# Optimization experiments

Measured on AMD Instinct MI355X. Metric: run time of the kernel, lower is better.

The kernel has to match this reference:

```python
import jax, jax.numpy as jnp
import numpy as np

B, T, D = 2, 2048, 1024
E, K, FF = 8, 2, 4096


def setup_inputs() -> dict:
    key = jax.random.key(0)
    ks = jax.random.split(key, 4)
    scale = 0.02
    return {
        "x": jax.random.normal(ks[0], (B, T, D), jnp.float32),
        "gate_w": jax.random.normal(ks[1], (D, E), jnp.float32) * scale,
        "gate_b": jnp.zeros((E,), jnp.float32),
        "w1": jax.random.normal(ks[2], (E, D, FF), jnp.float32) * scale,
        "b1": jnp.zeros((E, FF), jnp.float32),
        "w2": jax.random.normal(ks[3], (E, FF, D), jnp.float32) * scale,
        "b2": jnp.zeros((E, D), jnp.float32),
    }


def reference(x, gate_w, gate_b, w1, b1, w2, b2):
    # x: (B,T,D). Original runs every expert densely over all tokens then masks;
    # since mask*x == x at selected positions and output is re-masked, the math
    # equals: output[t] = sum_k softmax(topk_vals)[k] * expert_{idx_k}(x)[t].
    n_experts = w1.shape[0]
    gate_logits = x @ gate_w + gate_b                      # (B,T,E)
    topk_vals, topk_idx = jax.lax.top_k(gate_logits, K)    # (B,T,K)
    topk_w = jax.nn.softmax(topk_vals, axis=-1)            # (B,T,K)
    onehot = jax.nn.one_hot(topk_idx, n_experts, dtype=x.dtype)  # (B,T,K,E)
    comb = jnp.sum(onehot * topk_w[..., None], axis=2)     # (B,T,E) combine weights

    # Dense per-expert FFN over all tokens (faithful to original redundant compute)
    h = jax.nn.gelu(jnp.einsum('btd,edf->ebtf', x, w1) + b1[:, None, None, :],
                    approximate=False)                      # (E,B,T,FF)
    y = jnp.einsum('ebtf,efd->ebtd', h, w2) + b2[:, None, None, :]  # (E,B,T,D)
    output = jnp.einsum('ebtd,bte->btd', y, comb)           # (B,T,D)

    expert_counts = jnp.sum(onehot, axis=(0, 1, 2)).astype(jnp.float32)  # (E,)
    return output, gate_logits, topk_idx, expert_counts
```

## Files before the change

kernel.cpp:

```cpp
#include <hip/hip_runtime.h>
#include <math.h>

#define NTOK 4096
#define DIM  1024
#define NE   8
#define FF   4096

#define OUT_LOGITS 4194304
#define OUT_IDX    4227072
#define OUT_CNT    4235264

typedef unsigned short u16;
typedef __bf16 bf16x8 __attribute__((ext_vector_type(8)));
typedef float  f32x4  __attribute__((ext_vector_type(4)));
typedef u16    u16x8  __attribute__((ext_vector_type(8)));

__device__ __forceinline__ u16 f2bf(float f) {
  union { float f; unsigned u; } v; v.f = f;
  unsigned r = v.u + 0x7fffu + ((v.u >> 16) & 1u);
  return (u16)(r >> 16);
}

__device__ __forceinline__ float gelu_f(float v) {
  float u = v * (0.7978845608f + 0.0356774081f * v * v);
  float e = __expf(2.f * u);
  float t = 1.f - 2.f / (e + 1.f);
  return 0.5f * v * (1.f + t);
}

__device__ __forceinline__ void gload_lds16(const u16* g, u16* l) {
  __builtin_amdgcn_global_load_lds(
      (const __attribute__((address_space(1))) void*)(g),
      (__attribute__((address_space(3))) void*)(l), 16, 0, 0);
}

__global__ __launch_bounds__(256) void transpose_cvt2_kernel(
    const float* __restrict__ w1, u16* __restrict__ w1t,
    const float* __restrict__ w2, u16* __restrict__ w2t) {
  __shared__ float tile[4096];
  int id = blockIdx.x;
  const float* in; u16* out; int R, C, xt, yt, z;
  if (id < 8192) {
    in = w1; out = w1t; R = DIM; C = FF;
    xt = id & 63; yt = (id >> 6) & 15; z = id >> 10;
  } else {
    int i2 = id - 8192;
    in = w2; out = w2t; R = FF; C = DIM;
    xt = i2 & 15; yt = (i2 >> 4) & 63; z = i2 >> 10;
  }
  in  += (size_t)z * R * C;
  out += (size_t)z * R * C;
  const int c0 = xt * 64, r0 = yt * 64;
  const int t = threadIdx.x;

  {
    int cc = t & 15, rr = t >> 4;
    #pragma unroll
    for (int p = 0; p < 4; p++) {
      int r = rr + p * 16;
      float4 v = *(const float4*)(in + (size_t)(r0 + r) * C + c0 + cc * 4);
      *(float4*)&tile[r * 64 + ((cc ^ (r >> 3)) << 2)] = v;
    }
  }
  __syncthreads();
  {
    int h = t & 7, cg = t >> 3;
    #pragma unroll
    for (int p = 0; p < 2; p++) {
      int c = p * 32 + cg;
      int base = ((((c >> 2) ^ h) << 2)) + (c & 3);
      u16x8 o;
      #pragma unroll
      for (int j = 0; j < 8; j++)
        o[j] = f2bf(tile[(h * 8 + j) * 64 + base]);
      *(u16x8*)(out + (size_t)(c0 + c) * R + r0 + h * 8) = o;
    }
  }
}

__global__ __launch_bounds__(256) void gate_kernel(const float* __restrict__ x,
                                                   const float* __restrict__ gw,
                                                   const float* __restrict__ gb,
                                                   float* __restrict__ out,
                                                   int2* __restrict__ tk_idx,
                                                   float2* __restrict__ tk_w) {
  int wave = threadIdx.x >> 6, lane = threadIdx.x & 63;
  int token = blockIdx.x * 4 + wave;
  const float* xr = x + (size_t)token * DIM + lane * 16;
  float acc[NE];
  #pragma unroll
  for (int e = 0; e < NE; e++) acc[e] = 0.f;
  #pragma unroll
  for (int c = 0; c < 16; c += 4) {
    float4 xv = *(const float4*)(xr + c);
    const float* gwr = gw + (size_t)(lane * 16 + c) * NE;
    float xs[4] = {xv.x, xv.y, xv.z, xv.w};
    #pragma unroll
    for (int q = 0; q < 4; q++)
      #pragma unroll
      for (int e = 0; e < NE; e++)
        acc[e] += xs[q] * gwr[q * NE + e];
  }
  #pragma unroll
  for (int off = 32; off; off >>= 1)
    #pragma unroll
    for (int e = 0; e < NE; e++)
      acc[e] += __shfl_down(acc[e], off);

  if (lane == 0) {
    float lg[NE];
    #pragma unroll
    for (int e = 0; e < NE; e++) {
      lg[e] = acc[e] + gb[e];
      out[OUT_LOGITS + token * NE + e] = lg[e];
    }
    int i0 = 0; float v0 = lg[0];
    #pragma unroll
    for (int e = 1; e < NE; e++) if (lg[e] > v0) { v0 = lg[e]; i0 = e; }
    int i1 = -1; float v1 = -1e30f;
    #pragma unroll
    for (int e = 0; e < NE; e++) if (e != i0 && lg[e] > v1) { v1 = lg[e]; i1 = e; }
    float ex = expf(v1 - v0);
    float s = 1.f + ex;
    out[OUT_IDX + token * 2]     = (float)i0;
    out[OUT_IDX + token * 2 + 1] = (float)i1;
    tk_idx[token] = make_int2(i0, i1);
    tk_w[token]   = make_float2(1.f / s, ex / s);
  }
}

__global__ __launch_bounds__(512) void build_lists_kernel(
    const int2* __restrict__ tk_idx, const float2* __restrict__ tk_w,
    int* __restrict__ counts, int* __restrict__ offsets,
    int* __restrict__ tok_list, float* __restrict__ wt_list,
    float* __restrict__ cnt_out) {
  __shared__ int s_cnt[NE];
  int e = threadIdx.x >> 6, lane = threadIdx.x & 63;
  int cnt = 0;
  for (int base = 0; base < NTOK; base += 64) {
    int2 idx = tk_idx[base + lane];
    cnt += __popcll(__ballot(idx.x == e || idx.y == e));
  }
  if (lane == 0) s_cnt[e] = cnt;
  __syncthreads();
  int off = 0;
  for (int ee = 0; ee < e; ee++) off += s_cnt[ee];
  if (lane == 0) {
    counts[e]  = s_cnt[e];
    offsets[e] = off;
    cnt_out[e] = (float)s_cnt[e];
  }
  int pos = off;
  for (int base = 0; base < NTOK; base += 64) {
    int tok = base + lane;
    int2 idx = tk_idx[tok];
    float2 w = tk_w[tok];
    bool m0 = (idx.x == e), m1 = (idx.y == e);
    bool m = m0 || m1;
    unsigned long long mask = __ballot(m);
    if (m) {
      int p = pos + __popcll(mask & ((1ull << lane) - 1ull));
      tok_list[p] = tok;
      wt_list[p]  = m0 ? w.x : w.y;
    }
    pos += __popcll(mask);
  }
}

__global__ __launch_bounds__(256) void gather_x_kernel(const float* __restrict__ x,
                                                       const int* __restrict__ tok_list,
                                                       u16* __restrict__ xg) {
  int g = blockIdx.x;
  int tok = tok_list[g];
  int c = threadIdx.x * 4;
  float4 v = *(const float4*)(x + (size_t)tok * DIM + c);
  ushort4 o;
  o.x = f2bf(v.x); o.y = f2bf(v.y); o.z = f2bf(v.z); o.w = f2bf(v.w);
  *(ushort4*)(xg + (size_t)g * DIM + c) = o;
}

template <int MODE, int BM, int BN>
__global__ __launch_bounds__(512, 2) void moe_gemm2_kernel(
    const u16* __restrict__ Abase, const u16* __restrict__ Bbase,
    const float* __restrict__ bias,
    const int* __restrict__ counts, const int* __restrict__ offsets,
    const int* __restrict__ tok_list, const float* __restrict__ wt_list,
    u16* __restrict__ Hout, float* __restrict__ Out) {
  constexpr int KT = (MODE == 0) ? DIM : FF;
  constexpr int NT = (MODE == 0) ? FF : DIM;
  constexpr int LA = BM / 64;
  constexpr int LB = BN / 64;
  constexpr int MR = BM / 32;
  constexpr int NR = BN / 64;
  constexpr int ASZ = BM * 64;
  constexpr int BSZ = BN * 64;
  constexpr int NTILES = (MODE == 0) ? (KT / 64) : (KT / 128);

  extern __shared__ u16 sm[];

  const int zz = blockIdx.z;
  const int e  = (MODE == 1) ? (zz >> 1) : zz;
  const int koff = (MODE == 1) ? ((zz & 1) * (KT / 2)) : 0;
  const int ne = counts[e];
  const int m0 = blockIdx.y * BM;
  if (m0 >= ne) return;
  const int n0   = blockIdx.x * BN;
  const int offs = offsets[e];

  const int t = threadIdx.x;
  const int wave = t >> 6, lane = t & 63;
  const int quad = lane >> 4, l16 = lane & 15;
  const int wmb = (wave & 1) * (BM / 2);
  const int wnb = (wave >> 1) * (BN / 4);

  const u16* aptr[LA];
  const u16* bptr[LB];
  #pragma unroll
  for (int p = 0; p < LA; p++) {
    int idx = p * 512 + t;
    int row = idx >> 3, c = idx & 7;
    int clog = c ^ (row & 7);
    int s = m0 + row; if (s > ne - 1) s = ne - 1;
    aptr[p] = Abase + (size_t)(offs + s) * KT + koff + clog * 8;
  }
  #pragma unroll
  for (int p = 0; p < LB; p++) {
    int idx = p * 512 + t;
    int row = idx >> 3, c = idx & 7;
    int clog = c ^ (row & 7);
    bptr[p] = Bbase + ((size_t)e * NT + n0 + row) * KT + koff + clog * 8;
  }

  auto stage = [&](int buf, int k0) {
    #pragma unroll
    for (int p = 0; p < LA; p++)
      gload_lds16(aptr[p] + k0, sm + buf * ASZ + (p * 512 + t) * 8);
    #pragma unroll
    for (int p = 0; p < LB; p++)
      gload_lds16(bptr[p] + k0, sm + 2 * ASZ + buf * BSZ + (p * 512 + t) * 8);
  };

  const int xrow = l16 & 7;
  const int xo[2] = { ((0 + quad) ^ xrow) * 8, ((4 + quad) ^ xrow) * 8 };
  const int abase0 = (wmb + l16) * 64;
  const int bbase0 = 2 * ASZ + (wnb + l16) * 64;

  f32x4 acc[MR][NR];
  #pragma unroll
  for (int i = 0; i < MR; i++)
    #pragma unroll
    for (int j = 0; j < NR; j++)
      acc[i][j] = (f32x4){0.f, 0.f, 0.f, 0.f};

  stage(0, 0);
  __syncthreads();
  int cur = 0;
  for (int kt = 0; kt < NTILES; ++kt) {
    if (kt + 1 < NTILES) stage(cur ^ 1, (kt + 1) * 64);
    const u16* As = sm + cur * ASZ;
    const u16* Bs = sm + cur * BSZ;
    #pragma unroll
    for (int kk = 0; kk < 2; kk++) {
      bf16x8 a[MR], b[NR];
      #pragma unroll
      for (int i = 0; i < MR; i++) a[i] = *(const bf16x8*)&As[abase0 + i * 1024 + xo[kk]];
      #pragma unroll
      for (int j = 0; j < NR; j++) b[j] = *(const bf16x8*)&Bs[bbase0 + j * 1024 + xo[kk]];
      #pragma unroll
      for (int i = 0; i < MR; i++)
        #pragma unroll
        for (int j = 0; j < NR; j++)
          acc[i][j] = __builtin_amdgcn_mfma_f32_16x16x32_bf16(a[i], b[j], acc[i][j], 0, 0, 0);
    }
    __syncthreads();
    cur ^= 1;
  }

  if (MODE == 0) {
    const float* bb = bias + (size_t)e * FF + n0 + wnb;
    float bc[NR];
    #pragma unroll
    for (int j = 0; j < NR; j++) bc[j] = bb[j * 16 + l16];
    #pragma unroll
    for (int i = 0; i < MR; i++) {
      #pragma unroll
      for (int r = 0; r < 4; r++) {
        int s = m0 + wmb + i * 16 + quad * 4 + r;
        if (s < ne) {
          u16* hr = Hout + (size_t)(offs + s) * FF + n0 + wnb;
          #pragma unroll
          for (int j = 0; j < NR; j++)
            hr[j * 16 + l16] = f2bf(gelu_f(acc[i][j][r] + bc[j]));
        }
      }
    }
  } else {
    const float* bb = bias + (size_t)e * DIM + n0 + wnb;
    float bc[NR];
    #pragma unroll
    for (int j = 0; j < NR; j++) bc[j] = (zz & 1) ? 0.f : bb[j * 16 + l16];
    #pragma unroll
    for (int i = 0; i < MR; i++) {
      #pragma unroll
      for (int r = 0; r < 4; r++) {
        int s = m0 + wmb + i * 16 + quad * 4 + r;
        if (s < ne) {
          int   tok = tok_list[offs + s];
          float w   = wt_list[offs + s];
          float* orow = Out + (size_t)tok * DIM + n0 + wnb;
          #pragma unroll
          for (int j = 0; j < NR; j++)
            atomicAdd(&orow[j * 16 + l16], (acc[i][j][r] + bc[j]) * w);
        }
      }
    }
  }
}

extern "C" void kernel_launch(void* const* d_in, const int* in_sizes, int n_in,
                              void* d_out, int out_size, void* d_ws, size_t ws_size,
                              hipStream_t stream) {
  const float* x   = (const float*)d_in[0];
  const float* gw  = (const float*)d_in[1];
  const float* gb  = (const float*)d_in[2];
  const float* w1  = (const float*)d_in[3];
  const float* b1  = (const float*)d_in[4];
  const float* w2  = (const float*)d_in[5];
  const float* b2  = (const float*)d_in[6];
  float* out = (float*)d_out;
  char*  ws  = (char*)d_ws;

  u16* w1t = (u16*)(ws);
  u16* w2t = (u16*)(ws + 1ull * 67108864);
  u16* h   = (u16*)(ws + 2ull * 67108864);
  u16* xg  = (u16*)(ws + 3ull * 67108864);
  char* meta = ws + 3ull * 67108864 + 16777216;
  int*    counts   = (int*)(meta);
  int*    offsets  = (int*)(meta + 64);
  int*    tok_list = (int*)(meta + 128);
  float*  wt_list  = (float*)(meta + 128 + 32768);
  int2*   tk_idx   = (int2*)(meta + 128 + 2 * 32768);
  float2* tk_w     = (float2*)(meta + 128 + 2 * 32768 + 32768);
  (void)in_sizes; (void)n_in; (void)out_size; (void)ws_size;

  static bool attr_set = false;
  if (!attr_set) {
    hipFuncSetAttribute(reinterpret_cast<const void*>(moe_gemm2_kernel<0, 256, 256>),
                        hipFuncAttributeMaxDynamicSharedMemorySize, 131072);
    hipFuncSetAttribute(reinterpret_cast<const void*>(moe_gemm2_kernel<1, 128, 256>),
                        hipFuncAttributeMaxDynamicSharedMemorySize, 98304);
    attr_set = true;
  }

  hipMemsetAsync(out, 0, (size_t)OUT_LOGITS * 4, stream);

  transpose_cvt2_kernel<<<16384, 256, 0, stream>>>(w1, w1t, w2, w2t);
  gate_kernel<<<NTOK / 4, 256, 0, stream>>>(x, gw, gb, out, tk_idx, tk_w);
  build_lists_kernel<<<1, 512, 0, stream>>>(tk_idx, tk_w, counts, offsets, tok_list, wt_list,
                                            out + OUT_CNT);
  gather_x_kernel<<<2 * NTOK, 256, 0, stream>>>(x, tok_list, xg);

  moe_gemm2_kernel<0, 256, 256><<<dim3(FF / 256, NTOK / 256, NE), 512, 131072, stream>>>(
      xg, w1t, b1, counts, offsets, tok_list, wt_list, h, nullptr);
  moe_gemm2_kernel<1, 128, 256><<<dim3(DIM / 256, NTOK / 128, NE * 2), 512, 98304, stream>>>(
      h, w2t, b2, counts, offsets, tok_list, wt_list, nullptr, out);
}
```

Baseline: 636.3 us.

## Enlarge transpose tiles, parallelize list building, drop split-K in second GEMM

Three separate changes. The weight transpose/convert kernel now handles 128-row tiles per block, halving the block count. The token-list builder runs one block per expert, with each wave counting a slice of tokens, instead of a single block scanning all tokens serially. The down-projection GEMM no longer splits K across two z-slices, which halves its grid and its atomicAdd traffic but leaves fewer blocks and longer K loops per block.

```diff
diff --git a/kernel.cpp b/kernel.cpp
--- a/kernel.cpp
+++ b/kernel.cpp
@@ -34,29 +34,29 @@
       (__attribute__((address_space(3))) void*)(l), 16, 0, 0);
 }
 
-__global__ __launch_bounds__(256) void transpose_cvt2_kernel(
+__global__ __launch_bounds__(256) void transpose_cvt3_kernel(
     const float* __restrict__ w1, u16* __restrict__ w1t,
     const float* __restrict__ w2, u16* __restrict__ w2t) {
-  __shared__ float tile[4096];
+  __shared__ float tile[8192];
   int id = blockIdx.x;
   const float* in; u16* out; int R, C, xt, yt, z;
-  if (id < 8192) {
+  if (id < 4096) {
     in = w1; out = w1t; R = DIM; C = FF;
-    xt = id & 63; yt = (id >> 6) & 15; z = id >> 10;
+    xt = id & 63; yt = (id >> 6) & 7; z = id >> 9;
   } else {
-    int i2 = id - 8192;
+    int i2 = id - 4096;
     in = w2; out = w2t; R = FF; C = DIM;
-    xt = i2 & 15; yt = (i2 >> 4) & 63; z = i2 >> 10;
+    xt = i2 & 15; yt = (i2 >> 4) & 31; z = i2 >> 9;
   }
   in  += (size_t)z * R * C;
   out += (size_t)z * R * C;
-  const int c0 = xt * 64, r0 = yt * 64;
+  const int c0 = xt * 64, r0 = yt * 128;
   const int t = threadIdx.x;
 
   {
     int cc = t & 15, rr = t >> 4;
     #pragma unroll
-    for (int p = 0; p < 4; p++) {
+    for (int p = 0; p < 8; p++) {
       int r = rr + p * 16;
       float4 v = *(const float4*)(in + (size_t)(r0 + r) * C + c0 + cc * 4);
       *(float4*)&tile[r * 64 + ((cc ^ (r >> 3)) << 2)] = v;
@@ -64,11 +64,12 @@
   }
   __syncthreads();
   {
-    int h = t & 7, cg = t >> 3;
-    #pragma unroll
-    for (int p = 0; p < 2; p++) {
-      int c = p * 32 + cg;
-      int base = ((((c >> 2) ^ h) << 2)) + (c & 3);
+    int h = t & 15, cg = t >> 4;
+    #pragma unroll
+    for (int q = 0; q < 4; q++) {
+      int c = q * 16 + cg;
+      int phys = ((q * 4 + (cg >> 2)) ^ h) << 2;
+      int base = phys + (cg & 3);
       u16x8 o;
       #pragma unroll
       for (int j = 0; j < 8; j++)
@@ -129,39 +130,59 @@
   }
 }
 
-__global__ __launch_bounds__(512) void build_lists_kernel(
+__global__ __launch_bounds__(512) void build_lists8_kernel(
     const int2* __restrict__ tk_idx, const float2* __restrict__ tk_w,
     int* __restrict__ counts, int* __restrict__ offsets,
     int* __restrict__ tok_list, float* __restrict__ wt_list,
     float* __restrict__ cnt_out) {
-  __shared__ int s_cnt[NE];
-  int e = threadIdx.x >> 6, lane = threadIdx.x & 63;
-  int cnt = 0;
-  for (int base = 0; base < NTOK; base += 64) {
-    int2 idx = tk_idx[base + lane];
-    cnt += __popcll(__ballot(idx.x == e || idx.y == e));
-  }
-  if (lane == 0) s_cnt[e] = cnt;
+  __shared__ int s_cnt[8][NE];
+  const int e = blockIdx.x;
+  const int w = threadIdx.x >> 6, lane = threadIdx.x & 63;
+  const int tbase = w * 512;
+  int cnt[NE];
+  #pragma unroll
+  for (int ee = 0; ee < NE; ee++) cnt[ee] = 0;
+  #pragma unroll
+  for (int it = 0; it < 8; it++) {
+    int2 idx = tk_idx[tbase + it * 64 + lane];
+    #pragma unroll
+    for (int ee = 0; ee < NE; ee++)
+      cnt[ee] += __popcll(__ballot(idx.x == ee || idx.y == ee));
+  }
+  if (lane == 0) {
+    #pragma unroll
+    for (int ee = 0; ee < NE; ee++) s_cnt[w][ee] = cnt[ee];
+  }
   __syncthreads();
+  int total[NE];
+  #pragma unroll
+  for (int ee = 0; ee < NE; ee++) {
+    int s = 0;
+    #pragma unroll
+    for (int ww = 0; ww < 8; ww++) s += s_cnt[ww][ee];
+    total[ee] = s;
+  }
   int off = 0;
-  for (int ee = 0; ee < e; ee++) off += s_cnt[ee];
-  if (lane == 0) {
-    counts[e]  = s_cnt[e];
+  for (int ee = 0; ee < e; ee++) off += total[ee];
+  if (threadIdx.x == 0) {
+    counts[e]  = total[e];
     offsets[e] = off;
-    cnt_out[e] = (float)s_cnt[e];
+    cnt_out[e] = (float)total[e];
   }
   int pos = off;
-  for (int base = 0; base < NTOK; base += 64) {
-    int tok = base + lane;
+  for (int ww = 0; ww < w; ww++) pos += s_cnt[ww][e];
+  #pragma unroll
+  for (int it = 0; it < 8; it++) {
+    int tok = tbase + it * 64 + lane;
     int2 idx = tk_idx[tok];
-    float2 w = tk_w[tok];
+    float2 wt = tk_w[tok];
     bool m0 = (idx.x == e), m1 = (idx.y == e);
     bool m = m0 || m1;
     unsigned long long mask = __ballot(m);
     if (m) {
       int p = pos + __popcll(mask & ((1ull << lane) - 1ull));
       tok_list[p] = tok;
-      wt_list[p]  = m0 ? w.x : w.y;
+      wt_list[p]  = m0 ? wt.x : wt.y;
     }
     pos += __popcll(mask);
   }
@@ -194,13 +215,11 @@
   constexpr int NR = BN / 64;
   constexpr int ASZ = BM * 64;
   constexpr int BSZ = BN * 64;
-  constexpr int NTILES = (MODE == 0) ? (KT / 64) : (KT / 128);
+  constexpr int NTILES = KT / 64;
 
   extern __shared__ u16 sm[];
 
-  const int zz = blockIdx.z;
-  const int e  = (MODE == 1) ? (zz >> 1) : zz;
-  const int koff = (MODE == 1) ? ((zz & 1) * (KT / 2)) : 0;
+  const int e  = blockIdx.z;
   const int ne = counts[e];
   const int m0 = blockIdx.y * BM;
   if (m0 >= ne) return;
@@ -221,14 +240,14 @@
     int row = idx >> 3, c = idx & 7;
     int clog = c ^ (row & 7);
     int s = m0 + row; if (s > ne - 1) s = ne - 1;
-    aptr[p] = Abase + (size_t)(offs + s) * KT + koff + clog * 8;
+    aptr[p] = Abase + (size_t)(offs + s) * KT + clog * 8;
   }
   #pragma unroll
   for (int p = 0; p < LB; p++) {
     int idx = p * 512 + t;
     int row = idx >> 3, c = idx & 7;
     int clog = c ^ (row & 7);
-    bptr[p] = Bbase + ((size_t)e * NT + n0 + row) * KT + koff + clog * 8;
+    bptr[p] = Bbase + ((size_t)e * NT + n0 + row) * KT + clog * 8;
   }
 
   auto stage = [&](int buf, int k0) {
@@ -298,7 +317,7 @@
     const float* bb = bias + (size_t)e * DIM + n0 + wnb;
     float bc[NR];
     #pragma unroll
-    for (int j = 0; j < NR; j++) bc[j] = (zz & 1) ? 0.f : bb[j * 16 + l16];
+    for (int j = 0; j < NR; j++) bc[j] = bb[j * 16 + l16];
     #pragma unroll
     for (int i = 0; i < MR; i++) {
       #pragma unroll
@@ -354,14 +373,14 @@
 
   hipMemsetAsync(out, 0, (size_t)OUT_LOGITS * 4, stream);
 
-  transpose_cvt2_kernel<<<16384, 256, 0, stream>>>(w1, w1t, w2, w2t);
+  transpose_cvt3_kernel<<<8192, 256, 0, stream>>>(w1, w1t, w2, w2t);
   gate_kernel<<<NTOK / 4, 256, 0, stream>>>(x, gw, gb, out, tk_idx, tk_w);
-  build_lists_kernel<<<1, 512, 0, stream>>>(tk_idx, tk_w, counts, offsets, tok_list, wt_list,
-                                            out + OUT_CNT);
+  build_lists8_kernel<<<NE, 512, 0, stream>>>(tk_idx, tk_w, counts, offsets, tok_list, wt_list,
+                                              out + OUT_CNT);
   gather_x_kernel<<<2 * NTOK, 256, 0, stream>>>(x, tok_list, xg);
 
   moe_gemm2_kernel<0, 256, 256><<<dim3(FF / 256, NTOK / 256, NE), 512, 131072, stream>>>(
       xg, w1t, b1, counts, offsets, tok_list, wt_list, h, nullptr);
-  moe_gemm2_kernel<1, 128, 256><<<dim3(DIM / 256, NTOK / 128, NE * 2), 512, 98304, stream>>>(
+  moe_gemm2_kernel<1, 128, 256><<<dim3(DIM / 256, NTOK / 128, NE), 512, 98304, stream>>>(
       h, w2t, b2, counts, offsets, tok_list, wt_list, nullptr, out);
 }
```

New measurement: 606.3 us. 4.7% less time.
